# Optimization experiments

Measured on AMD Instinct MI355X. Metric: run time of the kernel, lower is better.

## Reference

```python
import jax, jax.numpy as jnp
import numpy as np

B, D = 32768, 1024


def setup_inputs() -> dict:
    key = jax.random.key(0)
    kx, k1, k2, k3 = jax.random.split(key, 4)
    x = jax.random.normal(kx, (B, D), dtype=jnp.float32)
    w1 = jax.random.normal(k1, (D, D), dtype=jnp.float32) * 0.1
    w2 = jax.random.normal(k2, (D, D), dtype=jnp.float32) * 0.1
    w3 = jax.random.normal(k3, (D, D), dtype=jnp.float32) * 0.1
    return {"x": x, "w1": w1, "w2": w2, "w3": w3}


def reference(x, w1, w2, w3):
    # Order 1: plain dense projection
    r1 = jnp.matmul(x, w1)  # [B, D]

    dim = x.shape[1]
    k = int(dim * 0.1)
    # Select top-k facets by mean |x| over the batch
    _, idx = jax.lax.top_k(jnp.abs(x).mean(axis=0), k)  # [k]
    mask = jnp.zeros((dim,), dtype=x.dtype).at[idx].set(1.0)  # [D]

    x_sparse = x * mask  # [B, D], zero outside active facets
    # Order 2: masked matmul, gated elementwise by the sparse input
    r2 = jnp.matmul(x_sparse, w2) * x_sparse
    # Order 3: masked matmul squared, gated elementwise
    r3 = jnp.square(jnp.matmul(x_sparse, w3)) * x_sparse
    return (r1, r2, r3)
```

## Files before the change

### kernel.cpp

```cpp
#include <hip/hip_runtime.h>
#include <hip/hip_bf16.h>
#include <stdint.h>

#define B_ROWS 32768
#define DIM    1024
#define KACT   102
#define KPAD   104

typedef short bf16x8 __attribute__((ext_vector_type(8)));
typedef float f32x4  __attribute__((ext_vector_type(4)));

__device__ __forceinline__ unsigned short f2bf(float f) {
  union { float f; unsigned u; } v; v.f = f;
  unsigned u = v.u;
  unsigned r = u + 0x7fffu + ((u >> 16) & 1u);
  return (unsigned short)(r >> 16);
}

#define GLDS(g, l) __builtin_amdgcn_global_load_lds( \
    (__attribute__((address_space(1))) void*)(g),    \
    (__attribute__((address_space(3))) void*)(l), 16, 0, 0)

__global__ __launch_bounds__(256) void k_conv(
    const float* __restrict__ x, unsigned short* __restrict__ xb,
    float* __restrict__ partial) {
  const int t  = threadIdx.x;
  const int c0 = t * 4;
  const size_t base = (size_t)blockIdx.x * 64 * DIM;
  float s0 = 0.f, s1 = 0.f, s2 = 0.f, s3 = 0.f;
  #pragma unroll 4
  for (int j = 0; j < 64; ++j) {
    size_t off = base + (size_t)j * DIM + c0;
    float4 v = *(const float4*)(x + off);
    s0 += fabsf(v.x); s1 += fabsf(v.y); s2 += fabsf(v.z); s3 += fabsf(v.w);
    ushort4 o;
    o.x = f2bf(v.x); o.y = f2bf(v.y); o.z = f2bf(v.z); o.w = f2bf(v.w);
    *(ushort4*)(xb + off) = o;
  }
  float4 p; p.x = s0; p.y = s1; p.z = s2; p.w = s3;
  *(float4*)(partial + (size_t)blockIdx.x * DIM + c0) = p;
}

__global__ __launch_bounds__(256) void k_w1t(const float* __restrict__ w1,
                                             unsigned short* __restrict__ w1t) {
  __shared__ unsigned short tile[64][65];
  const int t  = threadIdx.x;
  const int bx = blockIdx.x & 15;
  const int by = blockIdx.x >> 4;
  for (int e = t; e < 64 * 64; e += 256) {
    int r = e >> 6, c = e & 63;
    tile[r][c] = f2bf(w1[(size_t)(by * 64 + r) * DIM + bx * 64 + c]);
  }
  __syncthreads();
  for (int e = t; e < 64 * 64; e += 256) {
    int c = e >> 6, r = e & 63;
    w1t[(size_t)(bx * 64 + c) * DIM + by * 64 + r] = tile[r][c];
  }
}

__global__ __launch_bounds__(128) void k_reduce1(const float* __restrict__ partial,
                                                 float* __restrict__ p2) {
  const int c  = (blockIdx.x & 7) * 128 + threadIdx.x;
  const int ks = blockIdx.x >> 3;
  float s = 0.f;
  #pragma unroll 8
  for (int p = ks * 64; p < ks * 64 + 64; ++p) s += partial[(size_t)p * DIM + c];
  p2[ks * DIM + c] = s;
}

__global__ __launch_bounds__(256) void k_rank(const float* __restrict__ p2,
                                              int* __restrict__ flags) {
  __shared__ double sv[DIM];
  const int t = threadIdx.x;
  for (int e = t; e < DIM; e += 256) {
    double s = 0.0;
    #pragma unroll
    for (int ks = 0; ks < 8; ++ks) s += (double)p2[ks * DIM + e];
    sv[e] = s;
  }
  __syncthreads();
  const int d = blockIdx.x * 256 + t;
  const double sd = sv[d];
  int rank = 0;
  for (int j = 0; j < DIM; ++j) {
    double s = sv[j];
    rank += (s > sd || (s == sd && j < d)) ? 1 : 0;
  }
  flags[d] = (rank < KACT) ? 1 : 0;
}

__global__ __launch_bounds__(1024) void k_compact(const int* __restrict__ flags,
                                                  int* __restrict__ act,
                                                  int* __restrict__ cmap) {
  __shared__ int wcnt[16];
  const int d = threadIdx.x;
  const int f = flags[d];
  unsigned long long m = __ballot(f != 0);
  const int lane = d & 63, w = d >> 6;
  if (lane == 0) wcnt[w] = __popcll(m);
  __syncthreads();
  int off = 0;
  for (int i = 0; i < w; ++i) off += wcnt[i];
  int pos = off + __popcll(m & ((1ull << lane) - 1ull));
  cmap[d] = f ? pos : -1;
  if (f) act[pos] = d;
}

__global__ __launch_bounds__(128) void k_wsub(const float* __restrict__ w2,
                                              const float* __restrict__ w3,
                                              const int* __restrict__ act,
                                              float* __restrict__ W2sub,
                                              float* __restrict__ W3sub) {
  const int i = blockIdx.x;
  const int j = threadIdx.x;
  if (j >= KPAD) return;
  float v2 = 0.f, v3 = 0.f;
  if (i < KACT && j < KACT) {
    size_t o = (size_t)act[i] * DIM + act[j];
    v2 = w2[o]; v3 = w3[o];
  }
  W2sub[i * KPAD + j] = v2;
  W3sub[i * KPAD + j] = v3;
}

__global__ __launch_bounds__(256) void k_gemm_r1(const unsigned short* __restrict__ A,
                                                 const unsigned short* __restrict__ Bt,
                                                 float* __restrict__ C) {
  constexpr int K  = DIM;
  constexpr int NT = K / 32;
  __shared__ unsigned short As[2][128 * 32];
  __shared__ unsigned short Bs[2][128 * 32];
  const int t    = threadIdx.x;
  const int lane = t & 63;
  const int wave = t >> 6;
  const int wrow = wave >> 1;
  const int wcol = wave & 1;
  const int swz  = (blockIdx.x & 7) * 256 + (blockIdx.x >> 3);
  const int brow = swz >> 3;
  const int bcol = swz & 7;

  const unsigned short* Ab0 = A  + (size_t)brow * 128 * K;
  const unsigned short* Bb0 = Bt + (size_t)bcol * 128 * K;

  const int p0 = t, p1 = t + 256;
  const int r0 = p0 >> 2, c0 = (p0 & 3) ^ ((r0 >> 1) & 3);
  const int r1 = p1 >> 2, c1 = (p1 & 3) ^ ((r1 >> 1) & 3);
  const size_t so0 = (size_t)r0 * K + c0 * 8;
  const size_t so1 = (size_t)r1 * K + c1 * 8;

  const int kg = lane >> 4;
  const int la = lane & 15;
  int posA[4], posB[4];
  #pragma unroll
  for (int i = 0; i < 4; ++i) {
    int R = wrow * 64 + i * 16 + la;
    posA[i] = (R * 4 + (kg ^ ((R >> 1) & 3))) * 8;
    int Cc = wcol * 64 + i * 16 + la;
    posB[i] = (Cc * 4 + (kg ^ ((Cc >> 1) & 3))) * 8;
  }

  f32x4 acc[4][4];
  #pragma unroll
  for (int mi = 0; mi < 4; ++mi)
    #pragma unroll
    for (int ni = 0; ni < 4; ++ni)
      acc[mi][ni] = (f32x4){0.f, 0.f, 0.f, 0.f};

  auto stage = [&](int kt, int buf) {
    const int k0 = kt * 32;
    GLDS(Ab0 + so0 + k0, &As[buf][p0 * 8]);
    GLDS(Ab0 + so1 + k0, &As[buf][p1 * 8]);
    GLDS(Bb0 + so0 + k0, &Bs[buf][p0 * 8]);
    GLDS(Bb0 + so1 + k0, &Bs[buf][p1 * 8]);
  };

  stage(0, 0);
  #pragma unroll 2
  for (int kt = 0; kt < NT; ++kt) {
    __syncthreads();
    const int cur = kt & 1;
    if (kt + 1 < NT) stage(kt + 1, cur ^ 1);
    bf16x8 av[4], bv[4];
    #pragma unroll
    for (int i = 0; i < 4; ++i) av[i] = *(const bf16x8*)(&As[cur][posA[i]]);
    #pragma unroll
    for (int i = 0; i < 4; ++i) bv[i] = *(const bf16x8*)(&Bs[cur][posB[i]]);
    #pragma unroll
    for (int mi = 0; mi < 4; ++mi)
      #pragma unroll
      for (int ni = 0; ni < 4; ++ni)
        acc[mi][ni] = __builtin_amdgcn_mfma_f32_16x16x32_bf16(av[mi], bv[ni],
                                                              acc[mi][ni], 0, 0, 0);
  }

  const int orow = brow * 128 + wrow * 64 + (lane >> 4) * 4;
  const int ocol = bcol * 128 + wcol * 64 + la;
  #pragma unroll
  for (int mi = 0; mi < 4; ++mi)
    #pragma unroll
    for (int ni = 0; ni < 4; ++ni)
      #pragma unroll
      for (int r = 0; r < 4; ++r)
        C[(size_t)(orow + mi * 16 + r) * DIM + ocol + ni * 16] = acc[mi][ni][r];
}

__global__ __launch_bounds__(512) void k_r23(const float* __restrict__ x,
                                             const float* __restrict__ W2sub,
                                             const float* __restrict__ W3sub,
                                             const int* __restrict__ cmap,
                                             float* __restrict__ out2,
                                             float* __restrict__ out3) {
  __shared__ float W2s[KPAD * KPAD];
  __shared__ float W3s[KPAD * KPAD];
  __shared__ float xs[2][16 * KPAD];
  __shared__ float r2s[16 * KPAD];
  __shared__ float r3s[16 * KPAD];
  __shared__ int   cms[DIM];
  const int t    = threadIdx.x;
  const int row0 = blockIdx.x * 128;

  for (int e = t; e < KPAD * KPAD; e += 512) { W2s[e] = W2sub[e]; W3s[e] = W3sub[e]; }
  for (int e = t; e < DIM; e += 512) cms[e] = cmap[e];
  for (int e = t; e < 2 * 16 * KPAD; e += 512) ((float*)xs)[e] = 0.f;
  __syncthreads();

  const int  j   = t & 127;
  const int  rg  = (t >> 7) & 3;
  const bool jok = j < KACT;

  auto LOADR = [&](int ch, f32x4* ld) {
    const size_t base = (size_t)(row0 + ch * 16) * DIM;
    #pragma unroll
    for (int it = 0; it < 8; ++it) {
      int e = t + it * 512;
      int r = e >> 8, c4 = e & 255;
      ld[it] = *(const f32x4*)(x + base + (size_t)r * DIM + c4 * 4);
    }
  };
  auto XSW = [&](int buf, const f32x4* ld) {
    #pragma unroll
    for (int it = 0; it < 8; ++it) {
      int e = t + it * 512;
      int r = e >> 8, c4 = e & 255;
      #pragma unroll
      for (int q = 0; q < 4; ++q) {
        int m = cms[c4 * 4 + q];
        if (m >= 0) xs[buf][r * KPAD + m] = ld[it][q];
      }
    }
  };
  auto COMPUTE = [&](int buf) {
    if (jok) {
      float a2[4], a3[4];
      #pragma unroll
      for (int r = 0; r < 4; ++r) { a2[r] = 0.f; a3[r] = 0.f; }
      for (int i = 0; i < KPAD; i += 4) {
        float w2v[4], w3v[4];
        #pragma unroll
        for (int q = 0; q < 4; ++q) {
          w2v[q] = W2s[(i + q) * KPAD + j];
          w3v[q] = W3s[(i + q) * KPAD + j];
        }
        #pragma unroll
        for (int r = 0; r < 4; ++r) {
          f32x4 xv = *(const f32x4*)(&xs[buf][(rg * 4 + r) * KPAD + i]);
          a2[r] += xv[0] * w2v[0] + xv[1] * w2v[1] + xv[2] * w2v[2] + xv[3] * w2v[3];
          a3[r] += xv[0] * w3v[0] + xv[1] * w3v[1] + xv[2] * w3v[2] + xv[3] * w3v[3];
        }
      }
      #pragma unroll
      for (int r = 0; r < 4; ++r) {
        int rr = rg * 4 + r;
        float g = xs[buf][rr * KPAD + j];
        r2s[rr * KPAD + j] = a2[r] * g;
        r3s[rr * KPAD + j] = a3[r] * a3[r] * g;
      }
    }
  };
  auto WRITEOUT = [&](int ch) {
    const int r0 = row0 + ch * 16;
    const int c0 = (t & 255) * 4;
    const int rh = t >> 8;
    const int4 cm = *(const int4*)(&cms[c0]);
    #pragma unroll
    for (int k = 0; k < 8; ++k) {
      int r = rh + k * 2;
      const float* rr2 = &r2s[r * KPAD];
      const float* rr3 = &r3s[r * KPAD];
      float4 o2, o3;
      o2.x = (cm.x >= 0) ? rr2[cm.x] : 0.f;  o3.x = (cm.x >= 0) ? rr3[cm.x] : 0.f;
      o2.y = (cm.y >= 0) ? rr2[cm.y] : 0.f;  o3.y = (cm.y >= 0) ? rr3[cm.y] : 0.f;
      o2.z = (cm.z >= 0) ? rr2[cm.z] : 0.f;  o3.z = (cm.z >= 0) ? rr3[cm.z] : 0.f;
      o2.w = (cm.w >= 0) ? rr2[cm.w] : 0.f;  o3.w = (cm.w >= 0) ? rr3[cm.w] : 0.f;
      size_t oo = (size_t)(r0 + r) * DIM + c0;
      *(float4*)(out2 + oo) = o2;
      *(float4*)(out3 + oo) = o3;
    }
  };

  f32x4 ldA[8], ldB[8];
  LOADR(0, ldA);
  XSW(0, ldA);
  __syncthreads();
  for (int ch2 = 0; ch2 < 8; ch2 += 2) {
    if (ch2 + 1 < 8) LOADR(ch2 + 1, ldB);
    COMPUTE(0);
    __syncthreads();
    WRITEOUT(ch2);
    if (ch2 + 1 < 8) XSW(1, ldB);
    __syncthreads();
    if (ch2 + 2 < 8) LOADR(ch2 + 2, ldA);
    COMPUTE(1);
    __syncthreads();
    WRITEOUT(ch2 + 1);
    if (ch2 + 2 < 8) XSW(0, ldA);
    __syncthreads();
  }
}

extern "C" void kernel_launch(void* const* d_in, const int* in_sizes, int n_in,
                              void* d_out, int out_size, void* d_ws, size_t ws_size,
                              hipStream_t stream) {
  const float* x  = (const float*)d_in[0];
  const float* w1 = (const float*)d_in[1];
  const float* w2 = (const float*)d_in[2];
  const float* w3 = (const float*)d_in[3];

  float* out1 = (float*)d_out;
  float* out2 = out1 + (size_t)B_ROWS * DIM;
  float* out3 = out2 + (size_t)B_ROWS * DIM;

  char* ws = (char*)d_ws;
  unsigned short* xb     = (unsigned short*)ws;
  unsigned short* w1t    = (unsigned short*)(ws + 67108864);
  float*          partial= (float*)(ws + 69206016);
  float*          p2     = (float*)(ws + 71303168);
  int*            flags  = (int*)(ws + 71335936);
  int*            act    = (int*)(ws + 71340032);
  int*            cmap   = (int*)(ws + 71340544);
  float*          W2sub  = (float*)(ws + 71344640);
  float*          W3sub  = (float*)(ws + 71387904);

  k_conv    <<<dim3(512),  dim3(256),  0, stream>>>(x, xb, partial);
  k_w1t     <<<dim3(256),  dim3(256),  0, stream>>>(w1, w1t);
  k_reduce1 <<<dim3(64),   dim3(128),  0, stream>>>(partial, p2);
  k_rank    <<<dim3(4),    dim3(256),  0, stream>>>(p2, flags);
  k_compact <<<dim3(1),    dim3(1024), 0, stream>>>(flags, act, cmap);
  k_wsub    <<<dim3(KPAD), dim3(128),  0, stream>>>(w2, w3, act, W2sub, W3sub);
  k_gemm_r1 <<<dim3(2048), dim3(256),  0, stream>>>(xb, w1t, out1);
  k_r23     <<<dim3(256),  dim3(512),  0, stream>>>(x, W2sub, W3sub, cmap, out2, out3);
}
```

Baseline: 283.9 us.

## Rewrite r1 GEMM with 256x256 tiles and 4-stage ping-pong LDS pipeline

The bf16 r1 GEMM now uses 256x256 output tiles per 512-thread block instead of 128x128, with each wave computing 128x64. Global loads into LDS go through a 4-slot ring with explicit vmcnt waits. Each k-step is split into two half-phases separated by barriers, with s_setprio raised around the MFMA bursts. The intent is better data reuse per LDS load and overlap of global loads with matrix math. The cost is higher register and LDS pressure, one block per CU, and fragile hand-scheduled waits.

```diff
diff --git a/kernel.cpp b/kernel.cpp
--- a/kernel.cpp
+++ b/kernel.cpp
@@ -123,85 +123,113 @@
   W3sub[i * KPAD + j] = v3;
 }
 
-__global__ __launch_bounds__(256) void k_gemm_r1(const unsigned short* __restrict__ A,
-                                                 const unsigned short* __restrict__ Bt,
-                                                 float* __restrict__ C) {
-  constexpr int K  = DIM;
-  constexpr int NT = K / 32;
-  __shared__ unsigned short As[2][128 * 32];
-  __shared__ unsigned short Bs[2][128 * 32];
+#define VMW4 asm volatile("s_waitcnt vmcnt(4)" ::: "memory")
+#define VMW0 asm volatile("s_waitcnt vmcnt(0)" ::: "memory")
+#define NOP_ (void)0
+
+#define STAGE_A(KT) do { \
+  GLDS(Abase + (size_t)sr0 * 1024 + (KT) * 32 + sc0 * 8, &Asl[((KT)&3)*8192 + p0*8]); \
+  GLDS(Abase + (size_t)sr1 * 1024 + (KT) * 32 + sc1 * 8, &Asl[((KT)&3)*8192 + p1*8]); \
+} while (0)
+#define STAGE_B(KT) do { \
+  GLDS(Bbase + (size_t)sr0 * 1024 + (KT) * 32 + sc0 * 8, &Bsl[((KT)&3)*8192 + p0*8]); \
+  GLDS(Bbase + (size_t)sr1 * 1024 + (KT) * 32 + sc1 * 8, &Bsl[((KT)&3)*8192 + p1*8]); \
+} while (0)
+
+#define PH0(SLOT, STAGE_STMT) do { \
+  _Pragma("unroll") for (int i = 0; i < 4; ++i) \
+    areg[i] = *(const bf16x8*)(&Asl[(SLOT)*8192 + aoff0 + i * 512]); \
+  _Pragma("unroll") for (int i = 0; i < 4; ++i) \
+    breg[i] = *(const bf16x8*)(&Bsl[(SLOT)*8192 + boff0 + i * 512]); \
+  STAGE_STMT; \
+  __builtin_amdgcn_s_barrier(); \
+  __builtin_amdgcn_s_setprio(1); \
+  _Pragma("unroll") for (int mi = 0; mi < 4; ++mi) \
+  _Pragma("unroll") for (int ni = 0; ni < 4; ++ni) \
+    acc[mi][ni] = __builtin_amdgcn_mfma_f32_16x16x32_bf16(areg[mi], breg[ni], acc[mi][ni], 0, 0, 0); \
+  __builtin_amdgcn_s_setprio(0); \
+  __builtin_amdgcn_s_barrier(); \
+} while (0)
+
+#define PH1(SLOT, STAGE_STMT, WAIT_STMT) do { \
+  _Pragma("unroll") for (int i = 0; i < 4; ++i) \
+    areg[i] = *(const bf16x8*)(&Asl[(SLOT)*8192 + aoff0 + 2048 + i * 512]); \
+  STAGE_STMT; \
+  WAIT_STMT; \
+  __builtin_amdgcn_s_barrier(); \
+  __builtin_amdgcn_s_setprio(1); \
+  _Pragma("unroll") for (int mi = 0; mi < 4; ++mi) \
+  _Pragma("unroll") for (int ni = 0; ni < 4; ++ni) \
+    acc[4 + mi][ni] = __builtin_amdgcn_mfma_f32_16x16x32_bf16(areg[mi], breg[ni], acc[4 + mi][ni], 0, 0, 0); \
+  __builtin_amdgcn_s_setprio(0); \
+  __builtin_amdgcn_s_barrier(); \
+} while (0)
+
+__global__ __launch_bounds__(512, 1) void k_gemm_r1(
+    const unsigned short* __restrict__ A,
+    const unsigned short* __restrict__ Bt,
+    float* __restrict__ C) {
+  __shared__ unsigned short Asl[4 * 8192];
+  __shared__ unsigned short Bsl[4 * 8192];
+
   const int t    = threadIdx.x;
   const int lane = t & 63;
   const int wave = t >> 6;
-  const int wrow = wave >> 1;
-  const int wcol = wave & 1;
-  const int swz  = (blockIdx.x & 7) * 256 + (blockIdx.x >> 3);
-  const int brow = swz >> 3;
-  const int bcol = swz & 7;
-
-  const unsigned short* Ab0 = A  + (size_t)brow * 128 * K;
-  const unsigned short* Bb0 = Bt + (size_t)bcol * 128 * K;
-
-  const int p0 = t, p1 = t + 256;
-  const int r0 = p0 >> 2, c0 = (p0 & 3) ^ ((r0 >> 1) & 3);
-  const int r1 = p1 >> 2, c1 = (p1 & 3) ^ ((r1 >> 1) & 3);
-  const size_t so0 = (size_t)r0 * K + c0 * 8;
-  const size_t so1 = (size_t)r1 * K + c1 * 8;
-
-  const int kg = lane >> 4;
-  const int la = lane & 15;
-  int posA[4], posB[4];
+  const int wm   = wave >> 2;
+  const int wn   = wave & 3;
+  const int la   = lane & 15;
+  const int kg   = lane >> 4;
+  const int kgx  = kg ^ ((la >> 1) & 3);
+
+  const int swz  = (blockIdx.x & 7) * 64 + (blockIdx.x >> 3);
+  const int brow = swz >> 2;
+  const int bcol = swz & 3;
+
+  const unsigned short* Abase = A  + (size_t)brow * 256 * 1024;
+  const unsigned short* Bbase = Bt + (size_t)bcol * 256 * 1024;
+
+  const int p0 = t, p1 = t + 512;
+  const int q0 = p0 ^ ((p0 >> 3) & 3);
+  const int q1 = p1 ^ ((p1 >> 3) & 3);
+  const int sr0 = q0 >> 2, sc0 = q0 & 3;
+  const int sr1 = q1 >> 2, sc1 = q1 & 3;
+
+  const int aoff0 = (wm * 128 + la) * 32 + kgx * 8;
+  const int boff0 = (wn * 64  + la) * 32 + kgx * 8;
+
+  f32x4 acc[8][4];
   #pragma unroll
-  for (int i = 0; i < 4; ++i) {
-    int R = wrow * 64 + i * 16 + la;
-    posA[i] = (R * 4 + (kg ^ ((R >> 1) & 3))) * 8;
-    int Cc = wcol * 64 + i * 16 + la;
-    posB[i] = (Cc * 4 + (kg ^ ((Cc >> 1) & 3))) * 8;
-  }
-
-  f32x4 acc[4][4];
-  #pragma unroll
-  for (int mi = 0; mi < 4; ++mi)
+  for (int mi = 0; mi < 8; ++mi)
     #pragma unroll
     for (int ni = 0; ni < 4; ++ni)
       acc[mi][ni] = (f32x4){0.f, 0.f, 0.f, 0.f};
 
-  auto stage = [&](int kt, int buf) {
-    const int k0 = kt * 32;
-    GLDS(Ab0 + so0 + k0, &As[buf][p0 * 8]);
-    GLDS(Ab0 + so1 + k0, &As[buf][p1 * 8]);
-    GLDS(Bb0 + so0 + k0, &Bs[buf][p0 * 8]);
-    GLDS(Bb0 + so1 + k0, &Bs[buf][p1 * 8]);
-  };
-
-  stage(0, 0);
-  #pragma unroll 2
-  for (int kt = 0; kt < NT; ++kt) {
-    __syncthreads();
-    const int cur = kt & 1;
-    if (kt + 1 < NT) stage(kt + 1, cur ^ 1);
-    bf16x8 av[4], bv[4];
-    #pragma unroll
-    for (int i = 0; i < 4; ++i) av[i] = *(const bf16x8*)(&As[cur][posA[i]]);
-    #pragma unroll
-    for (int i = 0; i < 4; ++i) bv[i] = *(const bf16x8*)(&Bs[cur][posB[i]]);
-    #pragma unroll
-    for (int mi = 0; mi < 4; ++mi)
-      #pragma unroll
-      for (int ni = 0; ni < 4; ++ni)
-        acc[mi][ni] = __builtin_amdgcn_mfma_f32_16x16x32_bf16(av[mi], bv[ni],
-                                                              acc[mi][ni], 0, 0, 0);
-  }
-
-  const int orow = brow * 128 + wrow * 64 + (lane >> 4) * 4;
-  const int ocol = bcol * 128 + wcol * 64 + la;
+  bf16x8 areg[4], breg[4];
+
+  STAGE_A(0); STAGE_B(0); STAGE_A(1); STAGE_B(1);
+  VMW4;
+  __builtin_amdgcn_s_barrier();
+
+  for (int kt4 = 0; kt4 < 28; kt4 += 4) {
+    PH0(0, STAGE_A(kt4 + 2)); PH1(0, STAGE_B(kt4 + 2), VMW4);
+    PH0(1, STAGE_A(kt4 + 3)); PH1(1, STAGE_B(kt4 + 3), VMW4);
+    PH0(2, STAGE_A(kt4 + 4)); PH1(2, STAGE_B(kt4 + 4), VMW4);
+    PH0(3, STAGE_A(kt4 + 5)); PH1(3, STAGE_B(kt4 + 5), VMW4);
+  }
+  PH0(0, STAGE_A(30)); PH1(0, STAGE_B(30), VMW4);
+  PH0(1, STAGE_A(31)); PH1(1, STAGE_B(31), VMW4);
+  PH0(2, NOP_);        PH1(2, NOP_, VMW0);
+  PH0(3, NOP_);        PH1(3, NOP_, NOP_);
+
+  const int orow0 = brow * 256 + wm * 128 + (lane >> 4) * 4;
+  const int ocol0 = bcol * 256 + wn * 64 + la;
   #pragma unroll
-  for (int mi = 0; mi < 4; ++mi)
+  for (int mi = 0; mi < 8; ++mi)
     #pragma unroll
     for (int ni = 0; ni < 4; ++ni)
       #pragma unroll
       for (int r = 0; r < 4; ++r)
-        C[(size_t)(orow + mi * 16 + r) * DIM + ocol + ni * 16] = acc[mi][ni][r];
+        C[(size_t)(orow0 + mi * 16 + r) * DIM + ocol0 + ni * 16] = acc[mi][ni][r];
 }
 
 __global__ __launch_bounds__(512) void k_r23(const float* __restrict__ x,
@@ -347,6 +375,6 @@
   k_rank    <<<dim3(4),    dim3(256),  0, stream>>>(p2, flags);
   k_compact <<<dim3(1),    dim3(1024), 0, stream>>>(flags, act, cmap);
   k_wsub    <<<dim3(KPAD), dim3(128),  0, stream>>>(w2, w3, act, W2sub, W3sub);
-  k_gemm_r1 <<<dim3(2048), dim3(256),  0, stream>>>(xb, w1t, out1);
+  k_gemm_r1 <<<dim3(512),  dim3(512),  0, stream>>>(xb, w1t, out1);
   k_r23     <<<dim3(256),  dim3(512),  0, stream>>>(x, W2sub, W3sub, cmap, out2, out3);
 }
```

Measured after the change: 256.8 us. 1.11x faster.
